# Performance work log

Hardware: AMD Instinct MI355X
Metric: run time of the kernel (lower is better)

The kernel has to match this reference:

```python
import jax, jax.numpy as jnp
import numpy as np

D_MODEL = 1024
NUM_HEAD = 16
D_K = D_MODEL // NUM_HEAD


def setup_inputs() -> dict:
    key = jax.random.key(0)
    ks = jax.random.split(key, 9)
    s = 1.0 / np.sqrt(D_MODEL)
    x = jax.random.normal(ks[0], (2, 2048, D_MODEL), dtype=jnp.float32)
    Wq = jax.random.uniform(ks[1], (D_MODEL, D_MODEL), jnp.float32, -s, s)
    bq = jax.random.uniform(ks[2], (D_MODEL,), jnp.float32, -s, s)
    Wk = jax.random.uniform(ks[3], (D_MODEL, D_MODEL), jnp.float32, -s, s)
    bk = jax.random.uniform(ks[4], (D_MODEL,), jnp.float32, -s, s)
    Wv = jax.random.uniform(ks[5], (D_MODEL, D_MODEL), jnp.float32, -s, s)
    bv = jax.random.uniform(ks[6], (D_MODEL,), jnp.float32, -s, s)
    Wo = jax.random.uniform(ks[7], (D_MODEL, D_MODEL), jnp.float32, -s, s)
    bo = jax.random.uniform(ks[8], (D_MODEL,), jnp.float32, -s, s)
    return {"x": x, "Wq": Wq, "bq": bq, "Wk": Wk, "bk": bk,
            "Wv": Wv, "bv": bv, "Wo": Wo, "bo": bo}


def reference(x, Wq, bq, Wk, bk, Wv, bv, Wo, bo):
    b, n, d = x.shape
    h, dk = NUM_HEAD, D_K
    # Linear projections (torch Linear: x @ W.T + b)
    q = (x @ Wq.T + bq).reshape(b, n, h, dk).transpose(0, 2, 1, 3)  # [b,h,n,dk]
    k = (x @ Wk.T + bk).reshape(b, n, h, dk).transpose(0, 2, 1, 3)
    v = (x @ Wv.T + bv).reshape(b, n, h, dk).transpose(0, 2, 1, 3)
    scores = jnp.einsum('bhqd,bhkd->bhqk', q, k) / jnp.sqrt(jnp.float32(dk))
    attn = jax.nn.softmax(scores, axis=-1)  # [b,h,n,n]
    out = jnp.einsum('bhqk,bhkd->bhqd', attn, v)
    out = out.transpose(0, 2, 1, 3).reshape(b, n, d)
    return out @ Wo.T + bo
```

## Files before the change

kernel.cpp:

```cpp
#include <hip/hip_runtime.h>

#define BATCH   2
#define SEQ     2048
#define DMODEL  1024
#define NHEAD   16
#define DKH     64
#define MTOT    (BATCH*SEQ)
#define KDIM    DMODEL

#define XB    0u
#define WQB   (4u*1024u*1024u)
#define WKB   (5u*1024u*1024u)
#define WVB   (6u*1024u*1024u)
#define WOB   (7u*1024u*1024u)
#define QOFF  (8u*1024u*1024u)
#define KOFF  (12u*1024u*1024u)
#define VOFF  (16u*1024u*1024u)
#define OOFF  (20u*1024u*1024u)

typedef __bf16 bf16x8 __attribute__((ext_vector_type(8)));
typedef __bf16 bf16x4 __attribute__((ext_vector_type(4)));
typedef float  f32x4  __attribute__((ext_vector_type(4)));
typedef float  f32x16 __attribute__((ext_vector_type(16)));

__device__ __forceinline__ void async16(const __bf16* g, __bf16* l) {
  __builtin_amdgcn_global_load_lds(
      (const __attribute__((address_space(1))) void*)g,
      (__attribute__((address_space(3))) void*)l, 16, 0, 0);
}

__global__ __launch_bounds__(256) void cvt_fp32_bf16(
    const float* __restrict__ x,  const float* __restrict__ wq,
    const float* __restrict__ wk, const float* __restrict__ wv,
    const float* __restrict__ wo, __bf16* __restrict__ ws)
{
  const float* src; __bf16* dst; int n;
  switch (blockIdx.y) {
    case 0:  src = x;  dst = ws + XB;  n = 4 * 1024 * 1024; break;
    case 1:  src = wq; dst = ws + WQB; n = 1024 * 1024;     break;
    case 2:  src = wk; dst = ws + WKB; n = 1024 * 1024;     break;
    case 3:  src = wv; dst = ws + WVB; n = 1024 * 1024;     break;
    default: src = wo; dst = ws + WOB; n = 1024 * 1024;     break;
  }
  const int i = (blockIdx.x * 256 + threadIdx.x) * 8;
  if (i < n) {
    const float4 a = *(const float4*)(src + i);
    const float4 b = *(const float4*)(src + i + 4);
    bf16x8 o;
    o[0] = (__bf16)a.x; o[1] = (__bf16)a.y; o[2] = (__bf16)a.z; o[3] = (__bf16)a.w;
    o[4] = (__bf16)b.x; o[5] = (__bf16)b.y; o[6] = (__bf16)b.z; o[7] = (__bf16)b.w;
    *(bf16x8*)(dst + i) = o;
  }
}

__device__ __forceinline__ void gemm128_core(
    const __bf16* __restrict__ A, const __bf16* __restrict__ W,
    int m0, int n0, __bf16* lds, f32x4 (&acc)[4][4])
{
  __bf16* A_lds = lds;
  __bf16* B_lds = lds + 4096;
  const int t    = threadIdx.x;
  const int w    = t >> 6;
  const int lane = t & 63;
  const int ln15 = lane & 15;
  const int quad = lane >> 4;
  const int wr   = (w >> 1) << 6;
  const int wc   = (w & 1) << 6;

#pragma unroll
  for (int i = 0; i < 4; ++i)
#pragma unroll
    for (int j = 0; j < 4; ++j) acc[i][j] = (f32x4){0.f, 0.f, 0.f, 0.f};

  for (int kt = 0; kt < KDIM; kt += 32) {
    __syncthreads();
#pragma unroll
    for (int issue = 0; issue < 2; ++issue) {
      const int cbase = issue * 256 + (w << 6);
      const int c     = cbase + lane;
      const int row   = c >> 2;
      const int goff  = ((c & 3) ^ (row & 3)) << 3;
      async16(A + (size_t)(m0 + row) * KDIM + kt + goff, A_lds + cbase * 8);
      async16(W + (size_t)(n0 + row) * KDIM + kt + goff, B_lds + cbase * 8);
    }
    __syncthreads();

    bf16x8 af[4], bfr[4];
#pragma unroll
    for (int i = 0; i < 4; ++i) {
      const int row = wr + i * 16 + ln15;
      af[i] = *(const bf16x8*)&A_lds[row * 32 + ((quad ^ (row & 3)) << 3)];
    }
#pragma unroll
    for (int j = 0; j < 4; ++j) {
      const int row = wc + j * 16 + ln15;
      bfr[j] = *(const bf16x8*)&B_lds[row * 32 + ((quad ^ (row & 3)) << 3)];
    }
#pragma unroll
    for (int i = 0; i < 4; ++i)
#pragma unroll
      for (int j = 0; j < 4; ++j)
        acc[i][j] = __builtin_amdgcn_mfma_f32_16x16x32_bf16(af[i], bfr[j], acc[i][j], 0, 0, 0);
  }
}

__global__ __launch_bounds__(256) void qkv_gemm(
    const __bf16* __restrict__ X,
    const __bf16* __restrict__ Wq, const float* __restrict__ bq,
    const __bf16* __restrict__ Wk, const float* __restrict__ bk,
    const __bf16* __restrict__ Wv, const float* __restrict__ bv,
    __bf16* __restrict__ ws)
{
  __shared__ __align__(16) __bf16 lds[128 * 64];

  const int z = blockIdx.z;
  const __bf16* W    = (z == 0) ? Wq : (z == 1) ? Wk : Wv;
  const float*  bias = (z == 0) ? bq : (z == 1) ? bk : bv;
  __bf16* out = ws + ((z == 0) ? QOFF : (z == 1) ? KOFF : VOFF);
  const float scale = (z == 0) ? 0.125f * 1.44269504088896f : 1.0f;

  const int m0 = blockIdx.x * 128;
  const int n0 = blockIdx.y * 128;

  f32x4 acc[4][4];
  gemm128_core(X, W, m0, n0, lds, acc);

  const int t = threadIdx.x, w = t >> 6, lane = t & 63;
  const int ln15 = lane & 15, quad = lane >> 4;
  const int wr = (w >> 1) << 6, wc = (w & 1) << 6;

  float bj4[4];
#pragma unroll
  for (int j = 0; j < 4; ++j) bj4[j] = bias[n0 + wc + j * 16 + ln15];

  __syncthreads();
  __bf16* scr = lds + (w << 10);

  const int bb = m0 >> 11;
  const int s_base = (m0 & 2047) + wr;
  const int h = (n0 + wc) >> 6;

  if (z != 2) {
    const int rdrow = lane & 15, rdseg = lane >> 4;
#pragma unroll
    for (int i = 0; i < 4; ++i) {
#pragma unroll
      for (int j = 0; j < 4; ++j)
#pragma unroll
        for (int rr = 0; rr < 4; ++rr)
          scr[(quad * 4 + rr) * 64 + j * 16 + ln15] =
              (__bf16)((acc[i][j][rr] + bj4[j]) * scale);
      bf16x8 v0 = *(const bf16x8*)&scr[rdrow * 64 + rdseg * 16];
      bf16x8 v1 = *(const bf16x8*)&scr[rdrow * 64 + rdseg * 16 + 8];
      const int s = s_base + i * 16 + rdrow;
      __bf16* p = out + (((size_t)(bb * NHEAD + h)) * SEQ + s) * DKH + rdseg * 16;
      *(bf16x8*)p = v0;
      *(bf16x8*)&p[8] = v1;
    }
  } else {
#pragma unroll
    for (int i = 0; i < 4; ++i) {
#pragma unroll
      for (int j = 0; j < 4; ++j) {
        bf16x4 pk;
#pragma unroll
        for (int rr = 0; rr < 4; ++rr) pk[rr] = (__bf16)(acc[i][j][rr] + bj4[j]);
        *(bf16x4*)&scr[(j * 16 + ln15) * 16 + quad * 4] = pk;
      }
      bf16x8 c0 = *(const bf16x8*)&scr[lane * 16];
      bf16x8 c1 = *(const bf16x8*)&scr[lane * 16 + 8];
      __bf16* p = out + (((size_t)(bb * NHEAD + h)) * DKH + lane) * SEQ
                      + s_base + i * 16;
      *(bf16x8*)p = c0;
      *(bf16x8*)&p[8] = c1;
    }
  }
}

__global__ __launch_bounds__(256) void out_gemm(
    const __bf16* __restrict__ A, const __bf16* __restrict__ Wo,
    const float* __restrict__ bo, float* __restrict__ out)
{
  __shared__ __align__(16) __bf16 lds[128 * 64];

  const int m0 = blockIdx.x * 128;
  const int n0 = blockIdx.y * 128;

  f32x4 acc[4][4];
  gemm128_core(A, Wo, m0, n0, lds, acc);

  const int t = threadIdx.x, w = t >> 6, lane = t & 63;
  const int ln15 = lane & 15, quad = lane >> 4;
  const int wr = (w >> 1) << 6, wc = (w & 1) << 6;

  float bj4[4];
#pragma unroll
  for (int j = 0; j < 4; ++j) bj4[j] = bo[n0 + wc + j * 16 + ln15];

  __syncthreads();
  float* scr = (float*)lds + (w << 10);

  const int rdrow = lane & 15, rdseg = lane >> 4;
#pragma unroll
  for (int i = 0; i < 4; ++i) {
#pragma unroll
    for (int j = 0; j < 4; ++j) {
      f32x4 v;
#pragma unroll
      for (int rr = 0; rr < 4; ++rr) v[rr] = acc[i][j][rr] + bj4[j];
      *(f32x4*)&scr[(j * 16 + ln15) * 16 + quad * 4] = v;
    }
    const int m = m0 + wr + i * 16 + rdrow;
    float* p = out + (size_t)m * DMODEL + n0 + wc + rdseg * 16;
#pragma unroll
    for (int cc = 0; cc < 4; ++cc) {
      f32x4 v;
#pragma unroll
      for (int e = 0; e < 4; ++e)
        v[e] = scr[(rdseg * 16 + cc * 4 + e) * 16 + rdrow];
      *(f32x4*)&p[cc * 4] = v;
    }
  }
}

__global__ __launch_bounds__(128) void attn_kernel(
    const __bf16* __restrict__ Qb, const __bf16* __restrict__ Kb,
    const __bf16* __restrict__ Vtb, __bf16* __restrict__ Ob)
{
  __shared__ __align__(16) __bf16 Qs[64 * 64];
  __shared__ __align__(16) __bf16 Ks[64 * 64];
  __shared__ __align__(16) __bf16 Vs[64 * 64];
  __shared__ __align__(16) __bf16 Ps[2 * 32 * 64];

  const int t = threadIdx.x, w = t >> 6, lane = t & 63;
  const int ln31 = lane & 31, hl = lane >> 5;
  const int b = blockIdx.z, h = blockIdx.y, q0 = blockIdx.x * 64;
  const size_t bh = (size_t)(b * NHEAD + h);

  const __bf16* Qg = Qb + bh * SEQ * DKH + (size_t)q0 * DKH;
  const __bf16* Kg = Kb + bh * SEQ * DKH;
  const __bf16* Vg = Vtb + bh * DKH * SEQ;

#pragma unroll
  for (int issue = 0; issue < 4; ++issue) {
    const int cbase = issue * 128 + (w << 6);
    const int c = cbase + lane;
    const int row = c >> 3;
    const int goff = ((c & 7) ^ (row & 7)) << 3;
    async16(Qg + (size_t)row * DKH + goff, Qs + cbase * 8);
  }
  __syncthreads();

  const int qrow = (w << 5) + ln31;
  bf16x8 qf[4];
#pragma unroll
  for (int ks = 0; ks < 4; ++ks) {
    const int chunk = ((2 * ks + hl) ^ (qrow & 7));
    qf[ks] = *(const bf16x8*)&Qs[qrow * 64 + (chunk << 3)];
  }

  float l_lane = 0.f;
  f32x16 o0, o1;
#pragma unroll
  for (int r = 0; r < 16; ++r) { o0[r] = 0.f; o1[r] = 0.f; }

  __bf16* Pw = Ps + w * (32 * 64);

  for (int kt = 0; kt < SEQ; kt += 64) {
    __syncthreads();
#pragma unroll
    for (int issue = 0; issue < 4; ++issue) {
      const int cbase = issue * 128 + (w << 6);
      const int c = cbase + lane;
      const int row = c >> 3;
      const int goff = ((c & 7) ^ (row & 7)) << 3;
      async16(Kg + (size_t)(kt + row) * DKH + goff, Ks + cbase * 8);
      async16(Vg + (size_t)row * SEQ + kt + goff, Vs + cbase * 8);
    }
    __syncthreads();

    f32x16 s0, s1;
#pragma unroll
    for (int r = 0; r < 16; ++r) { s0[r] = 0.f; s1[r] = 0.f; }
#pragma unroll
    for (int ks = 0; ks < 4; ++ks) {
      const int r0 = ln31;
      const int r1 = 32 + ln31;
      const int c0 = (((2 * ks + hl) ^ (r0 & 7)) << 3);
      const int c1 = (((2 * ks + hl) ^ (r1 & 7)) << 3);
      bf16x8 kf0 = *(const bf16x8*)&Ks[r0 * 64 + c0];
      bf16x8 kf1 = *(const bf16x8*)&Ks[r1 * 64 + c1];
      s0 = __builtin_amdgcn_mfma_f32_32x32x16_bf16(kf0, qf[ks], s0, 0, 0, 0);
      s1 = __builtin_amdgcn_mfma_f32_32x32x16_bf16(kf1, qf[ks], s1, 0, 0, 0);
    }

#pragma unroll
    for (int kb = 0; kb < 2; ++kb) {
      const f32x16& s = kb ? s1 : s0;
#pragma unroll
      for (int rg = 0; rg < 4; ++rg) {
        bf16x4 pk;
#pragma unroll
        for (int rr = 0; rr < 4; ++rr) {
          const float pv = __builtin_amdgcn_exp2f(s[rg * 4 + rr]);
          l_lane += pv;
          pk[rr] = (__bf16)pv;
        }
        const int g = kb * 4 + rg;
        *(bf16x4*)&Pw[ln31 * 64 + ((g ^ (ln31 & 7)) << 3) + hl * 4] = pk;
      }
    }

#pragma unroll
    for (int ks = 0; ks < 4; ++ks) {
      const int pg = (2 * ks + hl) ^ (ln31 & 7);
      bf16x8 pf = *(const bf16x8*)&Pw[ln31 * 64 + (pg << 3)];
      const int v0 = ln31;
      const int v1 = 32 + ln31;
      const int c0 = (((2 * ks + hl) ^ (v0 & 7)) << 3);
      const int c1 = (((2 * ks + hl) ^ (v1 & 7)) << 3);
      bf16x8 vf0 = *(const bf16x8*)&Vs[v0 * 64 + c0];
      bf16x8 vf1 = *(const bf16x8*)&Vs[v1 * 64 + c1];
      o0 = __builtin_amdgcn_mfma_f32_32x32x16_bf16(pf, vf0, o0, 0, 0, 0);
      o1 = __builtin_amdgcn_mfma_f32_32x32x16_bf16(pf, vf1, o1, 0, 0, 0);
    }
  }

  l_lane += __shfl_xor(l_lane, 32);
  const float inv = 1.0f / l_lane;

#pragma unroll
  for (int r = 0; r < 16; ++r) {
    const int qi = (r & 3) + 8 * (r >> 2) + 4 * hl;
    const float iq = __shfl(inv, qi);
    const int q = q0 + (w << 5) + qi;
    __bf16* rowp = Ob + ((size_t)(b * SEQ + q)) * DMODEL + h * DKH;
    rowp[ln31]      = (__bf16)(o0[r] * iq);
    rowp[32 + ln31] = (__bf16)(o1[r] * iq);
  }
}

extern "C" void kernel_launch(void* const* d_in, const int* in_sizes, int n_in,
                              void* d_out, int out_size, void* d_ws, size_t ws_size,
                              hipStream_t stream)
{
  const float* x  = (const float*)d_in[0];
  const float* Wq = (const float*)d_in[1];
  const float* bq = (const float*)d_in[2];
  const float* Wk = (const float*)d_in[3];
  const float* bk = (const float*)d_in[4];
  const float* Wv = (const float*)d_in[5];
  const float* bv = (const float*)d_in[6];
  const float* Wo = (const float*)d_in[7];
  const float* bo = (const float*)d_in[8];
  float*  out = (float*)d_out;
  __bf16* ws  = (__bf16*)d_ws;

  cvt_fp32_bf16<<<dim3(2048, 5, 1), 256, 0, stream>>>(x, Wq, Wk, Wv, Wo, ws);

  qkv_gemm<<<dim3(MTOT / 128, DMODEL / 128, 3), 256, 0, stream>>>(
      ws + XB, ws + WQB, bq, ws + WKB, bk, ws + WVB, bv, ws);

  attn_kernel<<<dim3(SEQ / 64, NHEAD, BATCH), 128, 0, stream>>>(
      ws + QOFF, ws + KOFF, ws + VOFF, ws + OOFF);

  out_gemm<<<dim3(MTOT / 128, DMODEL / 128, 1), 256, 0, stream>>>(
      ws + OOFF, ws + WOB, bo, out);
}
```

Baseline: 210.7 us.

## Enlarge attention query tile to 128 and shrink out-GEMM tile to 64x128

The attention kernel now runs 4 waves per block over 128 query rows, so each K/V tile loaded into LDS is shared by twice as many queries and the grid is reordered with batch-head as the fast dimension. The output projection drops the shared 128x128 GEMM core for a dedicated 64x128 tile with a 32-wide K step, doubling the block count to improve CU occupancy. The trade-off is fewer attention blocks and more LDS per block, plus lower arithmetic reuse per block in the output GEMM.

```diff
diff --git a/kernel.cpp b/kernel.cpp
--- a/kernel.cpp
+++ b/kernel.cpp
@@ -181,69 +181,110 @@
     const __bf16* __restrict__ A, const __bf16* __restrict__ Wo,
     const float* __restrict__ bo, float* __restrict__ out)
 {
-  __shared__ __align__(16) __bf16 lds[128 * 64];
-
-  const int m0 = blockIdx.x * 128;
+  __shared__ __align__(16) __bf16 lds[6144];
+  __bf16* A_lds = lds;
+  __bf16* B_lds = lds + 2048;
+
+  const int m0 = blockIdx.x * 64;
   const int n0 = blockIdx.y * 128;
-
-  f32x4 acc[4][4];
-  gemm128_core(A, Wo, m0, n0, lds, acc);
 
   const int t = threadIdx.x, w = t >> 6, lane = t & 63;
   const int ln15 = lane & 15, quad = lane >> 4;
-  const int wr = (w >> 1) << 6, wc = (w & 1) << 6;
-
-  float bj4[4];
-#pragma unroll
-  for (int j = 0; j < 4; ++j) bj4[j] = bo[n0 + wc + j * 16 + ln15];
+
+  f32x4 acc[4][2];
+#pragma unroll
+  for (int i = 0; i < 4; ++i)
+#pragma unroll
+    for (int j = 0; j < 2; ++j) acc[i][j] = (f32x4){0.f, 0.f, 0.f, 0.f};
+
+  for (int kt = 0; kt < KDIM; kt += 32) {
+    __syncthreads();
+    {
+      const int c = (w << 6) + lane;
+      const int row = c >> 2;
+      const int goff = ((c & 3) ^ (row & 3)) << 3;
+      async16(A + (size_t)(m0 + row) * KDIM + kt + goff, A_lds + c * 8);
+    }
+#pragma unroll
+    for (int issue = 0; issue < 2; ++issue) {
+      const int cbase = issue * 256 + (w << 6);
+      const int c = cbase + lane;
+      const int row = c >> 2;
+      const int goff = ((c & 3) ^ (row & 3)) << 3;
+      async16(Wo + (size_t)(n0 + row) * KDIM + kt + goff, B_lds + cbase * 8);
+    }
+    __syncthreads();
+
+    bf16x8 af[4], bfr[2];
+#pragma unroll
+    for (int i = 0; i < 4; ++i) {
+      const int row = i * 16 + ln15;
+      af[i] = *(const bf16x8*)&A_lds[row * 32 + ((quad ^ (row & 3)) << 3)];
+    }
+#pragma unroll
+    for (int j = 0; j < 2; ++j) {
+      const int row = (w << 5) + j * 16 + ln15;
+      bfr[j] = *(const bf16x8*)&B_lds[row * 32 + ((quad ^ (row & 3)) << 3)];
+    }
+#pragma unroll
+    for (int i = 0; i < 4; ++i)
+#pragma unroll
+      for (int j = 0; j < 2; ++j)
+        acc[i][j] = __builtin_amdgcn_mfma_f32_16x16x32_bf16(af[i], bfr[j], acc[i][j], 0, 0, 0);
+  }
+
+  float bj2[2];
+#pragma unroll
+  for (int j = 0; j < 2; ++j) bj2[j] = bo[n0 + (w << 5) + j * 16 + ln15];
 
   __syncthreads();
-  float* scr = (float*)lds + (w << 10);
+  float* scrf = (float*)lds + (w << 9);
 
   const int rdrow = lane & 15, rdseg = lane >> 4;
 #pragma unroll
   for (int i = 0; i < 4; ++i) {
 #pragma unroll
-    for (int j = 0; j < 4; ++j) {
+    for (int j = 0; j < 2; ++j) {
       f32x4 v;
 #pragma unroll
-      for (int rr = 0; rr < 4; ++rr) v[rr] = acc[i][j][rr] + bj4[j];
-      *(f32x4*)&scr[(j * 16 + ln15) * 16 + quad * 4] = v;
-    }
-    const int m = m0 + wr + i * 16 + rdrow;
-    float* p = out + (size_t)m * DMODEL + n0 + wc + rdseg * 16;
-#pragma unroll
-    for (int cc = 0; cc < 4; ++cc) {
+      for (int rr = 0; rr < 4; ++rr) v[rr] = acc[i][j][rr] + bj2[j];
+      *(f32x4*)&scrf[(j * 16 + ln15) * 16 + quad * 4] = v;
+    }
+    const int m = m0 + i * 16 + rdrow;
+    float* p = out + (size_t)m * DMODEL + n0 + (w << 5) + rdseg * 8;
+#pragma unroll
+    for (int cc = 0; cc < 2; ++cc) {
       f32x4 v;
 #pragma unroll
       for (int e = 0; e < 4; ++e)
-        v[e] = scr[(rdseg * 16 + cc * 4 + e) * 16 + rdrow];
+        v[e] = scrf[(rdseg * 8 + cc * 4 + e) * 16 + rdrow];
       *(f32x4*)&p[cc * 4] = v;
     }
   }
 }
 
-__global__ __launch_bounds__(128) void attn_kernel(
+__global__ __launch_bounds__(256) void attn_kernel(
     const __bf16* __restrict__ Qb, const __bf16* __restrict__ Kb,
     const __bf16* __restrict__ Vtb, __bf16* __restrict__ Ob)
 {
-  __shared__ __align__(16) __bf16 Qs[64 * 64];
+  __shared__ __align__(16) __bf16 Qs[128 * 64];
   __shared__ __align__(16) __bf16 Ks[64 * 64];
   __shared__ __align__(16) __bf16 Vs[64 * 64];
-  __shared__ __align__(16) __bf16 Ps[2 * 32 * 64];
+  __shared__ __align__(16) __bf16 Ps[4 * 32 * 64];
 
   const int t = threadIdx.x, w = t >> 6, lane = t & 63;
   const int ln31 = lane & 31, hl = lane >> 5;
-  const int b = blockIdx.z, h = blockIdx.y, q0 = blockIdx.x * 64;
-  const size_t bh = (size_t)(b * NHEAD + h);
-
-  const __bf16* Qg = Qb + bh * SEQ * DKH + (size_t)q0 * DKH;
-  const __bf16* Kg = Kb + bh * SEQ * DKH;
-  const __bf16* Vg = Vtb + bh * DKH * SEQ;
+  const int bh = blockIdx.x;
+  const int q0 = blockIdx.y * 128;
+  const int b = bh >> 4, h = bh & 15;
+
+  const __bf16* Qg = Qb + (size_t)bh * SEQ * DKH + (size_t)q0 * DKH;
+  const __bf16* Kg = Kb + (size_t)bh * SEQ * DKH;
+  const __bf16* Vg = Vtb + (size_t)bh * DKH * SEQ;
 
 #pragma unroll
   for (int issue = 0; issue < 4; ++issue) {
-    const int cbase = issue * 128 + (w << 6);
+    const int cbase = issue * 256 + (w << 6);
     const int c = cbase + lane;
     const int row = c >> 3;
     const int goff = ((c & 7) ^ (row & 7)) << 3;
@@ -269,8 +310,8 @@
   for (int kt = 0; kt < SEQ; kt += 64) {
     __syncthreads();
 #pragma unroll
-    for (int issue = 0; issue < 4; ++issue) {
-      const int cbase = issue * 128 + (w << 6);
+    for (int issue = 0; issue < 2; ++issue) {
+      const int cbase = issue * 256 + (w << 6);
       const int c = cbase + lane;
       const int row = c >> 3;
       const int goff = ((c & 7) ^ (row & 7)) << 3;
@@ -361,9 +402,9 @@
   qkv_gemm<<<dim3(MTOT / 128, DMODEL / 128, 3), 256, 0, stream>>>(
       ws + XB, ws + WQB, bq, ws + WKB, bk, ws + WVB, bv, ws);
 
-  attn_kernel<<<dim3(SEQ / 64, NHEAD, BATCH), 128, 0, stream>>>(
+  attn_kernel<<<dim3(BATCH * NHEAD, SEQ / 128), 256, 0, stream>>>(
       ws + QOFF, ws + KOFF, ws + VOFF, ws + OOFF);
 
-  out_gemm<<<dim3(MTOT / 128, DMODEL / 128, 1), 256, 0, stream>>>(
+  out_gemm<<<dim3(MTOT / 64, DMODEL / 128), 256, 0, stream>>>(
       ws + OOFF, ws + WOB, bo, out);
 }
```

Measured after the change: 192.8 us. -8.5%, faster.
